# Performance work log

Measured on AMD Instinct MI355X. Metric: run time of the kernel, lower is better.

The kernel has to match this reference:

```python
import jax, jax.numpy as jnp
import numpy as np

N, E, B = 20000, 320000, 64
NODE_DIM, EDGE_DIM, H, T = 64, 32, 128, 256
L = 5            # propagation_depth
DELTA = 1.0      # avg_d['log']
N_AGG, N_SCAL = 4, 3


def _w(k, shape):
    return jax.random.normal(k, shape, jnp.float32) / np.sqrt(shape[-2])


def setup_inputs() -> dict:
    key = jax.random.key(0)
    ks = jax.random.split(key, 12)
    return {
        "node_feat": jax.random.normal(ks[0], (N, NODE_DIM), jnp.float32),
        "edge_feat": jax.random.normal(ks[1], (E, EDGE_DIM), jnp.float32),
        "W_in": _w(ks[2], (NODE_DIM, H)),
        "b_in": jnp.zeros((H,), jnp.float32),
        "pre_W": _w(ks[3], (L, 2 * H + EDGE_DIM, H)),
        "pre_b": jnp.zeros((L, H), jnp.float32),
        "post_W": _w(ks[4], (L, H + N_AGG * N_SCAL * H, H)),
        "post_b": jnp.zeros((L, H), jnp.float32),
        "out_W1": _w(ks[5], (3 * H, H)),
        "out_b1": jnp.zeros((H,), jnp.float32),
        "out_W2": _w(ks[6], (H, T)),
        "out_b2": jnp.zeros((T,), jnp.float32),
        "src": jax.random.randint(ks[7], (E,), 0, N),
        "dst": jax.random.randint(ks[8], (E,), 0, N),
        "node2graph": jnp.sort(jax.random.randint(ks[9], (N,), 0, B)),
    }


def _forward(node_feat, edge_feat, W_in, b_in, pre_W, pre_b, post_W, post_b,
             out_W1, out_b1, out_W2, out_b2, src, dst, node2graph):
    # input node MLP (Linear + ReLU)
    h = jax.nn.relu(node_feat @ W_in + b_in)                       # [N, H]

    # degree-based scalers (constant across layers)
    deg = jax.ops.segment_sum(jnp.ones((E,), h.dtype), dst, num_segments=N)
    has_edge = (deg > 0)[:, None]
    inv_deg = jnp.where(deg > 0, 1.0 / jnp.maximum(deg, 1.0), 0.0)[:, None]
    logd = jnp.log(deg + 1.0)
    amp = (logd / DELTA)[:, None]                                  # amplification
    att = jnp.where(logd > 0, DELTA / jnp.maximum(logd, 1e-12), 1.0)[:, None]

    def step(h, p):
        pW, pb, qW, qb = p
        # pretrans on concat(src feat, dst feat, edge feat)
        m_in = jnp.concatenate([h[src], h[dst], edge_feat], axis=-1)  # [E, 2H+De]
        m = jax.nn.relu(m_in @ pW + pb)                               # [E, H]
        # multi-aggregator gather
        s = jax.ops.segment_sum(m, dst, num_segments=N)
        mean = s * inv_deg
        mx = jnp.where(has_edge, jax.ops.segment_max(m, dst, num_segments=N), 0.0)
        mn = jnp.where(has_edge, jax.ops.segment_min(m, dst, num_segments=N), 0.0)
        agg = jnp.concatenate([mean, mx, mn, s], axis=-1)             # [N, 4H]
        scaled = jnp.concatenate([agg, agg * amp, agg * att], axis=-1)  # [N, 12H]
        # posttrans on concat(h, aggregated)
        h_new = jax.nn.relu(jnp.concatenate([h, scaled], axis=-1) @ qW + qb)
        return h + h_new, None                                        # residual

    h, _ = jax.lax.scan(step, h, (pre_W, pre_b, post_W, post_b))

    # multi-aggregator readout over graphs
    g_sum = jax.ops.segment_sum(h, node2graph, num_segments=B)
    g_cnt = jax.ops.segment_sum(jnp.ones((N, 1), h.dtype), node2graph, num_segments=B)
    g_mean = g_sum / jnp.maximum(g_cnt, 1.0)
    g_max = jnp.where(g_cnt > 0, jax.ops.segment_max(h, node2graph, num_segments=B), 0.0)
    readout = jnp.concatenate([g_mean, g_max, g_sum], axis=-1)        # [B, 3H]
    return jax.nn.relu(readout @ out_W1 + out_b1) @ out_W2 + out_b2   # [B, T]


def reference(node_feat, edge_feat, W_in, b_in, pre_W, pre_b, post_W, post_b,
              out_W1, out_b1, out_W2, out_b2, src, dst, node2graph):
    return _forward(node_feat, edge_feat, W_in, b_in, pre_W, pre_b, post_W, post_b,
                    out_W1, out_b1, out_W2, out_b2, src, dst, node2graph)
```

## Files before the change

kernel.cpp:

```cpp
#include <hip/hip_runtime.h>

#define H 128
#define NODE_DIM 64
#define EDGE_DIM 32
#define KPRE (2*H + EDGE_DIM)
#define KPOST (13*H)
#define T_OUT 256
#define L_DEPTH 5
#define POST_FRAGS (52*8*64)
#define Y_FRAGS (4*16*64)
#define EF_FRAGS (8*64)
#define RCH 8

typedef short short8v __attribute__((ext_vector_type(8)));
typedef float float4v __attribute__((ext_vector_type(4)));

__device__ __forceinline__ unsigned short f2bf(float x) {
    unsigned int b = __float_as_uint(x);
    return (unsigned short)((b + 0x7fffu + ((b >> 16) & 1u)) >> 16);
}
__device__ __forceinline__ float bf2f(unsigned short u) {
    return __uint_as_float((unsigned int)u << 16);
}

__global__ void k_input_mlp(const float* __restrict__ nf, const float* __restrict__ W,
                            const float* __restrict__ b, float* __restrict__ h,
                            unsigned short* __restrict__ h_bf, int N) {
    int gid = blockIdx.x * blockDim.x + threadIdx.x;
    int n = gid >> 7, c = gid & 127;
    if (n >= N) return;
    const float* nrow = nf + (size_t)n * NODE_DIM;
    float acc = 0.f;
#pragma unroll 8
    for (int k = 0; k < NODE_DIM; ++k)
        acc += nrow[k] * W[k * H + c];
    acc += b[c];
    acc = fmaxf(acc, 0.f);
    h[(size_t)n * H + c] = acc;
    h_bf[(size_t)n * H + c] = f2bf(acc);
}

__global__ void k_hist(const int* __restrict__ dst, int* __restrict__ deg_i, int E) {
    int e = blockIdx.x * blockDim.x + threadIdx.x;
    if (e < E) atomicAdd(&deg_i[dst[e]], 1);
}

__global__ __launch_bounds__(1024) void k_scan(const int* __restrict__ deg_i,
                                               int* __restrict__ row_start,
                                               int* __restrict__ cursor, int N) {
    __shared__ int part[1024];
    int t = threadIdx.x;
    int per = (N + 1023) / 1024;
    int base = t * per;
    int s = 0;
    for (int i = 0; i < per; ++i) {
        int idx = base + i;
        if (idx < N) s += deg_i[idx];
    }
    part[t] = s;
    __syncthreads();
    for (int off = 1; off < 1024; off <<= 1) {
        int v = (t >= off) ? part[t - off] : 0;
        __syncthreads();
        part[t] += v;
        __syncthreads();
    }
    int run = (t == 0) ? 0 : part[t - 1];
    for (int i = 0; i < per; ++i) {
        int idx = base + i;
        if (idx < N) {
            row_start[idx] = run;
            cursor[idx] = run;
            run += deg_i[idx];
        }
    }
    if (t == 1023) row_start[N] = run;
}

__global__ void k_sortscatter(const int* __restrict__ src, const int* __restrict__ dst,
                              int* __restrict__ cursor, int* __restrict__ es_src,
                              int* __restrict__ es_eid, int E) {
    int e = blockIdx.x * blockDim.x + threadIdx.x;
    if (e >= E) return;
    int pos = atomicAdd(&cursor[dst[e]], 1);
    es_src[pos] = src[e];
    es_eid[pos] = e;
}

__global__ void k_efsort(const float* __restrict__ ef, const int* __restrict__ es_eid,
                         unsigned short* __restrict__ efs_bf, int E) {
    int t = blockIdx.x * 256 + threadIdx.x;
    int p = t >> 2, q = t & 3;
    if (p >= E) return;
    int eid = es_eid[p];
    const float* sp = ef + (size_t)eid * EDGE_DIM + q * 8;
    float4 v0 = *(const float4*)sp;
    float4 v1 = *(const float4*)(sp + 4);
    short8v o;
    o[0] = (short)f2bf(v0.x); o[1] = (short)f2bf(v0.y);
    o[2] = (short)f2bf(v0.z); o[3] = (short)f2bf(v0.w);
    o[4] = (short)f2bf(v1.x); o[5] = (short)f2bf(v1.y);
    o[6] = (short)f2bf(v1.z); o[7] = (short)f2bf(v1.w);
    *(short8v*)(efs_bf + (size_t)p * EDGE_DIM + q * 8) = o;
}

__global__ void k_scalers(const int* __restrict__ deg_i, float* __restrict__ invd,
                          float* __restrict__ amp, float* __restrict__ att, int N) {
    int n = blockIdx.x * blockDim.x + threadIdx.x;
    if (n >= N) return;
    float d = (float)deg_i[n];
    invd[n] = (d > 0.f) ? (1.f / d) : 0.f;
    float ld = logf(d + 1.f);
    amp[n] = ld;
    att[n] = (d > 0.f) ? (1.f / ld) : 1.f;
}

__global__ void k_gbounds(const int* __restrict__ n2g, int* __restrict__ g_start,
                          int N, int B) {
    int n = blockIdx.x * 256 + threadIdx.x;
    if (n > N) return;
    int cur = (n < N) ? n2g[n] : B;
    int prev = (n == 0) ? -1 : n2g[n - 1];
    for (int g = prev + 1; g <= cur && g <= B; ++g)
        g_start[g] = n;
}

__global__ void k_wconv_all(const float* __restrict__ pre_W,
                            const float* __restrict__ post_W,
                            short* __restrict__ wf_y_all,
                            short* __restrict__ wf_post_all,
                            short* __restrict__ wf_ef_all) {
    const int wrow[13] = {0, 256, 384, 512, 768, 896, 1024, 1280, 1408, 1536, 128, 640, 1152};
    int t = blockIdx.x * 256 + threadIdx.x;
    if (t < L_DEPTH * POST_FRAGS) {
        int l = t / POST_FRAGS, tt = t - l * POST_FRAGS;
        const float* qW = post_W + (size_t)l * KPOST * H;
        int lane = tt & 63, fc = tt >> 6;
        int b = fc >> 5, ks = (fc >> 3) & 3, cb = fc & 7;
        int col = cb * 16 + (lane & 15);
        int k0 = wrow[b] + ks * 32 + ((lane >> 4) << 3);
        short8v o;
#pragma unroll
        for (int j = 0; j < 8; ++j)
            o[j] = (short)f2bf(qW[(size_t)(k0 + j) * H + col]);
        *(short8v*)(wf_post_all + (size_t)t * 8) = o;
        return;
    }
    t -= L_DEPTH * POST_FRAGS;
    if (t < L_DEPTH * Y_FRAGS) {
        int l = t / Y_FRAGS, tt = t - l * Y_FRAGS;
        const float* pW = pre_W + (size_t)l * KPRE * H;
        int lane = tt & 63, fc = tt >> 6;
        int kglob = fc >> 4, cb = fc & 15;
        int col = cb * 16 + (lane & 15);
        int k0 = kglob * 32 + ((lane >> 4) << 3);
        int rowoff = (col < 128) ? 0 : 128;
        int c = col & 127;
        short8v o;
#pragma unroll
        for (int j = 0; j < 8; ++j)
            o[j] = (short)f2bf(pW[(size_t)(rowoff + k0 + j) * H + c]);
        *(short8v*)(wf_y_all + (size_t)t * 8) = o;
        return;
    }
    t -= L_DEPTH * Y_FRAGS;
    if (t >= L_DEPTH * EF_FRAGS) return;
    int l = t / EF_FRAGS, tt = t - l * EF_FRAGS;
    int lane = tt & 63, cb = tt >> 6;
    int col = cb * 16 + (lane & 15);
    int k0 = (lane >> 4) << 3;
    const float* pW = pre_W + (size_t)l * KPRE * H;
    short8v o;
#pragma unroll
    for (int j = 0; j < 8; ++j)
        o[j] = (short)f2bf(pW[(size_t)(2 * H + k0 + j) * H + col]);
    *(short8v*)(wf_ef_all + (size_t)t * 8) = o;
}

__device__ __forceinline__ void efw_body(
    int blk, const unsigned short* __restrict__ efs_bf,
    const short* __restrict__ WfEf, unsigned short* __restrict__ EFW, int E,
    unsigned short (*buf)[16][128])
{
    int tid = threadIdx.x, lane = tid & 63, w = tid >> 6;
    int p0 = blk * 256 + w * 64;
    short8v bfr[8];
#pragma unroll
    for (int cb = 0; cb < 8; ++cb)
        bfr[cb] = *(const short8v*)(WfEf + (size_t)(cb * 64 + lane) * 8);
#pragma unroll
    for (int t4 = 0; t4 < 4; ++t4) {
        int rowb = p0 + t4 * 16;
        int ar = rowb + (lane & 15);
        short8v a = {};
        if (ar < E)
            a = *(const short8v*)(efs_bf + (size_t)ar * EDGE_DIM + ((lane >> 4) << 3));
        float4v acc[8];
#pragma unroll
        for (int cb = 0; cb < 8; ++cb)
            acc[cb] = __builtin_amdgcn_mfma_f32_16x16x32_bf16(
                a, bfr[cb], (float4v){0.f, 0.f, 0.f, 0.f}, 0, 0, 0);
#pragma unroll
        for (int cb = 0; cb < 8; ++cb)
#pragma unroll
            for (int r = 0; r < 4; ++r)
                buf[w][((lane >> 4) << 2) + r][cb * 16 + (lane & 15)] = f2bf(acc[cb][r]);
#pragma unroll
        for (int j = 0; j < 4; ++j) {
            int lr = (lane >> 4) + j * 4;
            int gr = rowb + lr;
            uint4 v = *(const uint4*)&buf[w][lr][(lane & 15) * 8];
            if (gr < E)
                *(uint4*)(EFW + (size_t)gr * H + (lane & 15) * 8) = v;
        }
    }
}

__global__ __launch_bounds__(256) void k_y0_fat(
    const unsigned short* __restrict__ h_bf, const short* __restrict__ Wf,
    unsigned short* __restrict__ Y1bf, unsigned short* __restrict__ Y2bf, int N,
    const unsigned short* __restrict__ efs_bf, const short* __restrict__ WfEf,
    unsigned short* __restrict__ EFW, int E, int nYBlocks)
{
    __shared__ __align__(16) short Xs[64 * 128];
    __shared__ __align__(16) unsigned short buf[4][16][128];
    if (blockIdx.x >= nYBlocks) {
        efw_body(blockIdx.x - nYBlocks, efs_bf, WfEf, EFW, E, buf);
        return;
    }
    int tid = threadIdx.x;
    int n0 = blockIdx.x * 64;
    int lane = tid & 63, wave = tid >> 6;
    float4v acc[16];
#pragma unroll
    for (int cb = 0; cb < 16; ++cb) acc[cb] = (float4v){0.f, 0.f, 0.f, 0.f};

    int rs = tid >> 4, c0 = (tid & 15) * 8;
#pragma unroll
    for (int j = 0; j < 4; ++j) {
        int r = rs + j * 16;
        int n = n0 + r;
        uint4 v = make_uint4(0, 0, 0, 0);
        if (n < N) v = *(const uint4*)(h_bf + (size_t)n * H + c0);
        *(uint4*)((char*)Xs + r * 256 + ((c0 * 2) ^ ((r & 7) << 4))) = v;
    }
    __syncthreads();
    int rloc = wave * 16 + (lane & 15);
    int swz = (rloc & 7) << 4;
#pragma unroll
    for (int ks = 0; ks < 4; ++ks) {
        int boff = rloc * 256 + (((ks * 64) + ((lane >> 4) << 4)) ^ swz);
        short8v a = *(short8v*)((char*)Xs + boff);
        const short* wp = Wf + ((size_t)(ks * 16) * 64 + lane) * 8;
#pragma unroll
        for (int cb = 0; cb < 16; ++cb) {
            short8v b = *(const short8v*)(wp + (size_t)cb * 512);
            acc[cb] = __builtin_amdgcn_mfma_f32_16x16x32_bf16(a, b, acc[cb], 0, 0, 0);
        }
    }
    int col0 = lane & 15;
    int row0 = wave * 16 + ((lane >> 4) << 2);
#pragma unroll
    for (int cb = 0; cb < 16; ++cb) {
        int col = cb * 16 + col0;
#pragma unroll
        for (int r = 0; r < 4; ++r) {
            int n = n0 + row0 + r;
            if (n < N) {
                if (col < 128) Y1bf[(size_t)n * H + col] = f2bf(acc[cb][r]);
                else           Y2bf[(size_t)n * H + (col - 128)] = f2bf(acc[cb][r]);
            }
        }
    }
}

__global__ __launch_bounds__(256) void k_edge_agg(
    const unsigned short* __restrict__ Y1bf, const unsigned short* __restrict__ Y2bf,
    const unsigned short* __restrict__ EFW, const float* __restrict__ pb,
    const int* __restrict__ es_src, const int* __restrict__ row_start,
    unsigned short* __restrict__ s_out, unsigned short* __restrict__ mx_out,
    unsigned short* __restrict__ mn_out, int N)
{
    int tid = threadIdx.x, lane = tid & 63, w = tid >> 6;
    int n = blockIdx.x * 4 + w;
    if (n >= N) return;
    int start = row_start[n], end = row_start[n + 1];
    bool any = end > start;
    unsigned int y2u = *(const unsigned int*)(Y2bf + (size_t)n * H + 2 * lane);
    float2 pbv = *(const float2*)(pb + 2 * lane);
    float y20 = bf2f((unsigned short)(y2u & 0xffffu)) + pbv.x;
    float y21 = bf2f((unsigned short)(y2u >> 16)) + pbv.y;
    float s0 = 0.f, s1 = 0.f;
    float mx0 = any ? -3.4e38f : 0.f, mx1 = any ? -3.4e38f : 0.f;
    float mn0 = any ? 3.4e38f : 0.f,  mn1 = any ? 3.4e38f : 0.f;
#pragma unroll 2
    for (int p = start; p < end; ++p) {
        int sn = __builtin_amdgcn_readfirstlane(es_src[p]);
        unsigned int y1u = *(const unsigned int*)(Y1bf + (size_t)sn * H + 2 * lane);
        unsigned int eu  = *(const unsigned int*)(EFW + (size_t)p * H + 2 * lane);
        float m0 = fmaxf(bf2f((unsigned short)(y1u & 0xffffu)) +
                         bf2f((unsigned short)(eu & 0xffffu)) + y20, 0.f);
        float m1 = fmaxf(bf2f((unsigned short)(y1u >> 16)) +
                         bf2f((unsigned short)(eu >> 16)) + y21, 0.f);
        s0 += m0; s1 += m1;
        mx0 = fmaxf(mx0, m0); mx1 = fmaxf(mx1, m1);
        mn0 = fminf(mn0, m0); mn1 = fminf(mn1, m1);
    }
    size_t o = (size_t)n * H + 2 * lane;
    *(unsigned int*)(s_out + o)  = (unsigned int)f2bf(s0)  | ((unsigned int)f2bf(s1)  << 16);
    *(unsigned int*)(mx_out + o) = (unsigned int)f2bf(mx0) | ((unsigned int)f2bf(mx1) << 16);
    *(unsigned int*)(mn_out + o) = (unsigned int)f2bf(mn0) | ((unsigned int)f2bf(mn1) << 16);
}

__global__ __launch_bounds__(256) void k_post_fat(
    float* __restrict__ h, unsigned short* __restrict__ h_bf,
    const unsigned short* __restrict__ s_in, const unsigned short* __restrict__ mx_in,
    const unsigned short* __restrict__ mn_in,
    const float* __restrict__ invd, const float* __restrict__ amp,
    const float* __restrict__ att,
    const short* __restrict__ Wf, const float* __restrict__ qb,
    const short* __restrict__ WfY, unsigned short* __restrict__ Y1bf,
    unsigned short* __restrict__ Y2bf, int doY, int N,
    const unsigned short* __restrict__ efs_bf, const short* __restrict__ WfEf,
    unsigned short* __restrict__ EFW, int E, int nPostBlocks)
{
    __shared__ __align__(16) short Xs[32 * 128];
    __shared__ __align__(16) unsigned short buf[4][16][128];
    if (blockIdx.x >= nPostBlocks) {
        efw_body(blockIdx.x - nPostBlocks, efs_bf, WfEf, EFW, E, buf);
        return;
    }
    int tid = threadIdx.x, lane = tid & 63, wave = tid >> 6;
    int rh = wave & 1, ch = wave >> 1;
    int n0 = blockIdx.x * 32;

    const unsigned short* const srcs[13] = {h_bf, mx_in, mn_in, s_in, mx_in, mn_in, s_in,
                                            mx_in, mn_in, s_in, s_in, s_in, s_in};
    const int grp_of[13] = {0, 0, 0, 0, 1, 1, 1, 2, 2, 2, 3, 4, 5};

    float4v acc[6][4];
#pragma unroll
    for (int g = 0; g < 6; ++g)
#pragma unroll
        for (int cb = 0; cb < 4; ++cb) acc[g][cb] = (float4v){0.f, 0.f, 0.f, 0.f};

    int arow = n0 + rh * 16 + (lane & 15);
    bool aok = arow < N;
    size_t abase = (size_t)arow * H + ((lane >> 4) << 3);

#pragma unroll
    for (int b = 0; b < 13; ++b) {
        const unsigned short* sp = srcs[b];
#pragma unroll
        for (int ks = 0; ks < 4; ++ks) {
            short8v a = {};
            if (aok) a = *(const short8v*)(sp + abase + ks * 32);
#pragma unroll
            for (int cb = 0; cb < 4; ++cb) {
                short8v bfrag = *(const short8v*)(
                    Wf + ((size_t)((b * 4 + ks) * 8 + ch * 4 + cb) * 64 + lane) * 8);
                acc[grp_of[b]][cb] =
                    __builtin_amdgcn_mfma_f32_16x16x32_bf16(a, bfrag, acc[grp_of[b]][cb], 0, 0, 0);
            }
        }
    }

    int col0 = lane & 15;
    int row0 = rh * 16 + ((lane >> 4) << 2);
    float s_invd[4], s_amp[4], s_att[4];
#pragma unroll
    for (int r = 0; r < 4; ++r) {
        int n = n0 + row0 + r;
        bool ok = n < N;
        s_invd[r] = ok ? invd[n] : 0.f;
        s_amp[r]  = ok ? amp[n]  : 0.f;
        s_att[r]  = ok ? att[n]  : 0.f;
    }
#pragma unroll
    for (int cb = 0; cb < 4; ++cb) {
        int col = (ch * 4 + cb) * 16 + col0;
        float bb = qb[col];
#pragma unroll
        for (int r = 0; r < 4; ++r) {
            int n = n0 + row0 + r;
            if (n < N) {
                float v = acc[0][cb][r]
                        + s_amp[r] * acc[1][cb][r] + s_att[r] * acc[2][cb][r]
                        + s_invd[r] * (acc[3][cb][r] + s_amp[r] * acc[4][cb][r]
                                       + s_att[r] * acc[5][cb][r]);
                size_t o = (size_t)n * H + col;
                float nv = h[o] + fmaxf(v + bb, 0.f);
                h[o] = nv;
                unsigned short us = f2bf(nv);
                h_bf[o] = us;
                if (doY) {
                    int rr = row0 + r;
                    *(short*)((char*)Xs + rr * 256 + ((col * 2) ^ ((rr & 7) << 4))) = (short)us;
                }
            }
        }
    }
    if (doY) {
        __syncthreads();
        float4v yacc[8];
#pragma unroll
        for (int i = 0; i < 8; ++i) yacc[i] = (float4v){0.f, 0.f, 0.f, 0.f};
#pragma unroll
        for (int t16 = 0; t16 < 2; ++t16) {
            int rloc = t16 * 16 + (lane & 15);
            int swz = (rloc & 7) << 4;
#pragma unroll
            for (int ks = 0; ks < 4; ++ks) {
                int boff = rloc * 256 + (((ks * 64) + ((lane >> 4) << 4)) ^ swz);
                short8v a = *(short8v*)((char*)Xs + boff);
#pragma unroll
                for (int cb = 0; cb < 4; ++cb) {
                    const short* wp = WfY + ((size_t)(ks * 16 + wave * 4 + cb) * 64 + lane) * 8;
                    short8v b = *(const short8v*)wp;
                    yacc[t16 * 4 + cb] =
                        __builtin_amdgcn_mfma_f32_16x16x32_bf16(a, b, yacc[t16 * 4 + cb], 0, 0, 0);
                }
            }
        }
#pragma unroll
        for (int t16 = 0; t16 < 2; ++t16) {
#pragma unroll
            for (int cb = 0; cb < 4; ++cb) {
                int col = (wave * 4 + cb) * 16 + col0;
                int r0 = t16 * 16 + ((lane >> 4) << 2);
#pragma unroll
                for (int r = 0; r < 4; ++r) {
                    int n = n0 + r0 + r;
                    if (n < N) {
                        unsigned short v = f2bf(yacc[t16 * 4 + cb][r]);
                        if (col < 128) Y1bf[(size_t)n * H + col] = v;
                        else           Y2bf[(size_t)n * H + (col - 128)] = v;
                    }
                }
            }
        }
    }
}

__global__ __launch_bounds__(256) void k_readout_part(
    const float* __restrict__ h, const int* __restrict__ g_start,
    float* __restrict__ psum, float* __restrict__ pmax, int B)
{
    __shared__ float rs[2][128], rm[2][128];
    int blk = blockIdx.x;
    int b = blk / RCH, chunk = blk % RCH;
    int tid = threadIdx.x;
    int c = tid & 127, half = tid >> 7;
    int g0 = g_start[b], g1 = g_start[b + 1];
    int cnt = g1 - g0;
    int per = (cnt + RCH - 1) / RCH;
    int n0 = g0 + chunk * per;
    int n1 = min(n0 + per, g1);
    float s = 0.f, m = -3.4e38f;
    for (int n = n0 + half; n < n1; n += 2) {
        float v = h[(size_t)n * H + c];
        s += v;
        m = fmaxf(m, v);
    }
    rs[half][c] = s;
    rm[half][c] = m;
    __syncthreads();
    if (tid < 128) {
        size_t o = ((size_t)b * RCH + chunk) * H + c;
        psum[o] = rs[0][c] + rs[1][c];
        pmax[o] = fmaxf(rm[0][c], rm[1][c]);
    }
}

__global__ __launch_bounds__(256) void k_readout_final2(
    const float* __restrict__ psum, const float* __restrict__ pmax,
    const int* __restrict__ g_start,
    const float* __restrict__ W1, const float* __restrict__ b1,
    const float* __restrict__ W2, const float* __restrict__ b2,
    float* __restrict__ out)
{
    __shared__ float xv[3 * H];
    __shared__ float hid[H];
    int b = blockIdx.x, tid = threadIdx.x;
    int cnt = g_start[b + 1] - g_start[b];
    if (tid < 128) {
        int c = tid;
        float s = 0.f, m = -3.4e38f;
#pragma unroll
        for (int j = 0; j < RCH; ++j) {
            size_t o = ((size_t)b * RCH + j) * H + c;
            s += psum[o];
            m = fmaxf(m, pmax[o]);
        }
        float rc = 1.f / fmaxf((float)cnt, 1.f);
        xv[c]         = s * rc;
        xv[H + c]     = (cnt > 0) ? m : 0.f;
        xv[2 * H + c] = s;
    }
    __syncthreads();
    if (tid < 128) {
        float acc = 0.f;
        for (int k = 0; k < 3 * H; ++k)
            acc += xv[k] * W1[k * H + tid];
        hid[tid] = fmaxf(acc + b1[tid], 0.f);
    }
    __syncthreads();
    float acc = 0.f;
#pragma unroll 8
    for (int k = 0; k < H; ++k)
        acc += hid[k] * W2[k * T_OUT + tid];
    out[(size_t)b * T_OUT + tid] = acc + b2[tid];
}

extern "C" void kernel_launch(void* const* d_in, const int* in_sizes, int n_in,
                              void* d_out, int out_size, void* d_ws, size_t ws_size,
                              hipStream_t stream) {
    const float* node_feat = (const float*)d_in[0];
    const float* edge_feat = (const float*)d_in[1];
    const float* W_in  = (const float*)d_in[2];
    const float* b_in  = (const float*)d_in[3];
    const float* pre_W = (const float*)d_in[4];
    const float* pre_b = (const float*)d_in[5];
    const float* post_W = (const float*)d_in[6];
    const float* post_b = (const float*)d_in[7];
    const float* out_W1 = (const float*)d_in[8];
    const float* out_b1 = (const float*)d_in[9];
    const float* out_W2 = (const float*)d_in[10];
    const float* out_b2 = (const float*)d_in[11];
    const int* src = (const int*)d_in[12];
    const int* dst = (const int*)d_in[13];
    const int* n2g = (const int*)d_in[14];

    int N = in_sizes[0] / NODE_DIM;
    int E = in_sizes[1] / EDGE_DIM;
    int B = out_size / T_OUT;
    float* out = (float*)d_out;

    float* ws = (float*)d_ws;
    float* h    = ws; ws += (size_t)N * H;
    float* invd = ws; ws += N;
    float* amp  = ws; ws += N;
    float* att  = ws; ws += N;
    float* psum = ws; ws += (size_t)B * RCH * H;
    float* pmax = ws; ws += (size_t)B * RCH * H;
    ws = (float*)(((uintptr_t)ws + 15) & ~(uintptr_t)15);
    unsigned short* h_bf  = (unsigned short*)ws;
    unsigned short* s_buf = h_bf  + (size_t)N * H;
    unsigned short* mx    = s_buf + (size_t)N * H;
    unsigned short* mn    = mx    + (size_t)N * H;
    unsigned short* Y1bf  = mn    + (size_t)N * H;
    unsigned short* Y2bf  = Y1bf  + (size_t)N * H;
    unsigned short* efs_bf = Y2bf + (size_t)N * H;
    unsigned short* EFW    = efs_bf + (size_t)E * EDGE_DIM;
    short* wf_post_all = (short*)(EFW + (size_t)E * H);
    short* wf_y_all    = wf_post_all + (size_t)L_DEPTH * POST_FRAGS * 8;
    short* wf_ef_all   = wf_y_all + (size_t)L_DEPTH * Y_FRAGS * 8;
    int* deg_i     = (int*)(wf_ef_all + (size_t)L_DEPTH * EF_FRAGS * 8);
    int* row_start = deg_i + N;
    int* cursor    = row_start + N + 1;
    int* es_src    = cursor + N;
    int* es_eid    = es_src + E;
    int* g_start   = es_eid + E;

    int nPostBlocks = (N + 31) / 32;
    int nEfBlocks   = (E + 255) / 256;
    int nYBlocks    = (N + 63) / 64;

    k_input_mlp<<<((size_t)N * H + 255) / 256, 256, 0, stream>>>(node_feat, W_in, b_in,
                                                                 h, h_bf, N);

    hipMemsetAsync(deg_i, 0, (size_t)N * sizeof(int), stream);
    k_hist<<<(E + 255) / 256, 256, 0, stream>>>(dst, deg_i, E);
    k_scan<<<1, 1024, 0, stream>>>(deg_i, row_start, cursor, N);
    k_sortscatter<<<(E + 255) / 256, 256, 0, stream>>>(src, dst, cursor, es_src, es_eid, E);
    k_efsort<<<((size_t)E * 4 + 255) / 256, 256, 0, stream>>>(edge_feat, es_eid, efs_bf, E);
    k_scalers<<<(N + 255) / 256, 256, 0, stream>>>(deg_i, invd, amp, att, N);
    k_gbounds<<<(N + 256) / 256, 256, 0, stream>>>(n2g, g_start, N, B);

    {
        int tot = L_DEPTH * (POST_FRAGS + Y_FRAGS + EF_FRAGS);
        k_wconv_all<<<(tot + 255) / 256, 256, 0, stream>>>(pre_W, post_W, wf_y_all,
                                                           wf_post_all, wf_ef_all);
    }

    k_y0_fat<<<nYBlocks + nEfBlocks, 256, 0, stream>>>(
        h_bf, wf_y_all, Y1bf, Y2bf, N, efs_bf, wf_ef_all, EFW, E, nYBlocks);

    for (int l = 0; l < L_DEPTH; ++l) {
        k_edge_agg<<<(N + 3) / 4, 256, 0, stream>>>(
            Y1bf, Y2bf, EFW, pre_b + (size_t)l * H,
            es_src, row_start, s_buf, mx, mn, N);
        int doY = (l < L_DEPTH - 1) ? 1 : 0;
        int grid = nPostBlocks + (doY ? nEfBlocks : 0);
        k_post_fat<<<grid, 256, 0, stream>>>(
            h, h_bf, s_buf, mx, mn, invd, amp, att,
            wf_post_all + (size_t)l * POST_FRAGS * 8, post_b + (size_t)l * H,
            doY ? (wf_y_all + (size_t)(l + 1) * Y_FRAGS * 8) : wf_y_all,
            Y1bf, Y2bf, doY, N,
            efs_bf, doY ? (wf_ef_all + (size_t)(l + 1) * EF_FRAGS * 8) : wf_ef_all,
            EFW, E, nPostBlocks);
    }

    k_readout_part<<<B * RCH, 256, 0, stream>>>(h, g_start, psum, pmax, B);
    k_readout_final2<<<B, 256, 0, stream>>>(psum, pmax, g_start,
                                            out_W1, out_b1, out_W2, out_b2, out);
}
```

Measured before the change: 647.7 us.

## Fuse edge aggregation into post-transform kernel with LDS staging and double-buffered Y/EFW

The per-layer edge aggregation kernel is merged into the post-transform kernel. Each block first computes the sum, max and min aggregates for its 32 nodes into swizzled LDS, then feeds those tiles straight into the MFMA post-GEMM. Because the fused kernel reads this layer's Y1/Y2/EFW while writing the next layer's, those buffers are double-buffered. This removes one launch per layer and the global write and re-read of the three aggregate arrays. In exchange, each block now does a serial per-node gather before its GEMM, and LDS use grows to 32 KB, which may lower occupancy.

```diff
diff --git a/kernel.cpp b/kernel.cpp
--- a/kernel.cpp
+++ b/kernel.cpp
@@ -274,68 +274,70 @@
     }
 }
 
-__global__ __launch_bounds__(256) void k_edge_agg(
+__global__ __launch_bounds__(256) void k_aggpost_fat(
+    float* __restrict__ h, unsigned short* __restrict__ h_bf,
     const unsigned short* __restrict__ Y1bf, const unsigned short* __restrict__ Y2bf,
     const unsigned short* __restrict__ EFW, const float* __restrict__ pb,
     const int* __restrict__ es_src, const int* __restrict__ row_start,
-    unsigned short* __restrict__ s_out, unsigned short* __restrict__ mx_out,
-    unsigned short* __restrict__ mn_out, int N)
-{
-    int tid = threadIdx.x, lane = tid & 63, w = tid >> 6;
-    int n = blockIdx.x * 4 + w;
-    if (n >= N) return;
-    int start = row_start[n], end = row_start[n + 1];
-    bool any = end > start;
-    unsigned int y2u = *(const unsigned int*)(Y2bf + (size_t)n * H + 2 * lane);
-    float2 pbv = *(const float2*)(pb + 2 * lane);
-    float y20 = bf2f((unsigned short)(y2u & 0xffffu)) + pbv.x;
-    float y21 = bf2f((unsigned short)(y2u >> 16)) + pbv.y;
-    float s0 = 0.f, s1 = 0.f;
-    float mx0 = any ? -3.4e38f : 0.f, mx1 = any ? -3.4e38f : 0.f;
-    float mn0 = any ? 3.4e38f : 0.f,  mn1 = any ? 3.4e38f : 0.f;
-#pragma unroll 2
-    for (int p = start; p < end; ++p) {
-        int sn = __builtin_amdgcn_readfirstlane(es_src[p]);
-        unsigned int y1u = *(const unsigned int*)(Y1bf + (size_t)sn * H + 2 * lane);
-        unsigned int eu  = *(const unsigned int*)(EFW + (size_t)p * H + 2 * lane);
-        float m0 = fmaxf(bf2f((unsigned short)(y1u & 0xffffu)) +
-                         bf2f((unsigned short)(eu & 0xffffu)) + y20, 0.f);
-        float m1 = fmaxf(bf2f((unsigned short)(y1u >> 16)) +
-                         bf2f((unsigned short)(eu >> 16)) + y21, 0.f);
-        s0 += m0; s1 += m1;
-        mx0 = fmaxf(mx0, m0); mx1 = fmaxf(mx1, m1);
-        mn0 = fminf(mn0, m0); mn1 = fminf(mn1, m1);
-    }
-    size_t o = (size_t)n * H + 2 * lane;
-    *(unsigned int*)(s_out + o)  = (unsigned int)f2bf(s0)  | ((unsigned int)f2bf(s1)  << 16);
-    *(unsigned int*)(mx_out + o) = (unsigned int)f2bf(mx0) | ((unsigned int)f2bf(mx1) << 16);
-    *(unsigned int*)(mn_out + o) = (unsigned int)f2bf(mn0) | ((unsigned int)f2bf(mn1) << 16);
-}
-
-__global__ __launch_bounds__(256) void k_post_fat(
-    float* __restrict__ h, unsigned short* __restrict__ h_bf,
-    const unsigned short* __restrict__ s_in, const unsigned short* __restrict__ mx_in,
-    const unsigned short* __restrict__ mn_in,
     const float* __restrict__ invd, const float* __restrict__ amp,
     const float* __restrict__ att,
     const short* __restrict__ Wf, const float* __restrict__ qb,
-    const short* __restrict__ WfY, unsigned short* __restrict__ Y1bf,
-    unsigned short* __restrict__ Y2bf, int doY, int N,
+    const short* __restrict__ WfY, unsigned short* __restrict__ Y1o,
+    unsigned short* __restrict__ Y2o, int doY, int N,
     const unsigned short* __restrict__ efs_bf, const short* __restrict__ WfEf,
-    unsigned short* __restrict__ EFW, int E, int nPostBlocks)
+    unsigned short* __restrict__ EFWo, int E, int nPostBlocks)
 {
-    __shared__ __align__(16) short Xs[32 * 128];
-    __shared__ __align__(16) unsigned short buf[4][16][128];
+    __shared__ __align__(16) char smem[32768];
     if (blockIdx.x >= nPostBlocks) {
-        efw_body(blockIdx.x - nPostBlocks, efs_bf, WfEf, EFW, E, buf);
+        efw_body(blockIdx.x - nPostBlocks, efs_bf, WfEf, EFWo, E,
+                 (unsigned short (*)[16][128])smem);
         return;
     }
+    unsigned short* Ss  = (unsigned short*)smem;
+    unsigned short* Smx = Ss + 32 * 128;
+    unsigned short* Smn = Smx + 32 * 128;
+    short* Xs = (short*)(Smn + 32 * 128);
+
     int tid = threadIdx.x, lane = tid & 63, wave = tid >> 6;
+    int n0 = blockIdx.x * 32;
+
+#pragma unroll 1
+    for (int j = 0; j < 8; ++j) {
+        int r = wave * 8 + j;
+        int n = n0 + r;
+        float s0 = 0.f, s1 = 0.f, mx0 = 0.f, mx1 = 0.f, mn0 = 0.f, mn1 = 0.f;
+        if (n < N) {
+            int start = row_start[n], end = row_start[n + 1];
+            bool any = end > start;
+            unsigned int y2u = *(const unsigned int*)(Y2bf + (size_t)n * H + 2 * lane);
+            float2 pbv = *(const float2*)(pb + 2 * lane);
+            float y20 = bf2f((unsigned short)(y2u & 0xffffu)) + pbv.x;
+            float y21 = bf2f((unsigned short)(y2u >> 16)) + pbv.y;
+            mx0 = any ? -3.4e38f : 0.f; mx1 = mx0;
+            mn0 = any ? 3.4e38f : 0.f;  mn1 = mn0;
+#pragma unroll 2
+            for (int p = start; p < end; ++p) {
+                int sn = __builtin_amdgcn_readfirstlane(es_src[p]);
+                unsigned int y1u = *(const unsigned int*)(Y1bf + (size_t)sn * H + 2 * lane);
+                unsigned int eu  = *(const unsigned int*)(EFW + (size_t)p * H + 2 * lane);
+                float m0 = fmaxf(bf2f((unsigned short)(y1u & 0xffffu)) +
+                                 bf2f((unsigned short)(eu & 0xffffu)) + y20, 0.f);
+                float m1 = fmaxf(bf2f((unsigned short)(y1u >> 16)) +
+                                 bf2f((unsigned short)(eu >> 16)) + y21, 0.f);
+                s0 += m0; s1 += m1;
+                mx0 = fmaxf(mx0, m0); mx1 = fmaxf(mx1, m1);
+                mn0 = fminf(mn0, m0); mn1 = fminf(mn1, m1);
+            }
+        }
+        int boff = (r * 256 + lane * 4) ^ ((r & 7) << 4);
+        *(unsigned int*)((char*)Ss + boff)  = (unsigned int)f2bf(s0)  | ((unsigned int)f2bf(s1)  << 16);
+        *(unsigned int*)((char*)Smx + boff) = (unsigned int)f2bf(mx0) | ((unsigned int)f2bf(mx1) << 16);
+        *(unsigned int*)((char*)Smn + boff) = (unsigned int)f2bf(mn0) | ((unsigned int)f2bf(mn1) << 16);
+    }
+    __syncthreads();
+
     int rh = wave & 1, ch = wave >> 1;
-    int n0 = blockIdx.x * 32;
-
-    const unsigned short* const srcs[13] = {h_bf, mx_in, mn_in, s_in, mx_in, mn_in, s_in,
-                                            mx_in, mn_in, s_in, s_in, s_in, s_in};
+    const int src_of[13] = {0, 1, 2, 3, 1, 2, 3, 1, 2, 3, 3, 3, 3};
     const int grp_of[13] = {0, 0, 0, 0, 1, 1, 1, 2, 2, 2, 3, 4, 5};
 
     float4v acc[6][4];
@@ -344,17 +346,27 @@
 #pragma unroll
         for (int cb = 0; cb < 4; ++cb) acc[g][cb] = (float4v){0.f, 0.f, 0.f, 0.f};
 
-    int arow = n0 + rh * 16 + (lane & 15);
+    int arowL = rh * 16 + (lane & 15);
+    int arow = n0 + arowL;
     bool aok = arow < N;
     size_t abase = (size_t)arow * H + ((lane >> 4) << 3);
+    int lswz = (arowL & 7) << 4;
 
 #pragma unroll
     for (int b = 0; b < 13; ++b) {
-        const unsigned short* sp = srcs[b];
 #pragma unroll
         for (int ks = 0; ks < 4; ++ks) {
-            short8v a = {};
-            if (aok) a = *(const short8v*)(sp + abase + ks * 32);
+            short8v a;
+            if (src_of[b] == 0) {
+                short8v t = {};
+                if (aok) t = *(const short8v*)(h_bf + abase + ks * 32);
+                a = t;
+            } else {
+                const unsigned short* lp = (src_of[b] == 1) ? Smx
+                                          : (src_of[b] == 2) ? Smn : Ss;
+                int boff = (arowL * 256 + ks * 64 + ((lane >> 4) << 4)) ^ lswz;
+                a = *(const short8v*)((const char*)lp + boff);
+            }
 #pragma unroll
             for (int cb = 0; cb < 4; ++cb) {
                 short8v bfrag = *(const short8v*)(
@@ -364,6 +376,7 @@
             }
         }
     }
+    __syncthreads();
 
     int col0 = lane & 15;
     int row0 = rh * 16 + ((lane >> 4) << 2);
@@ -433,8 +446,8 @@
                     int n = n0 + r0 + r;
                     if (n < N) {
                         unsigned short v = f2bf(yacc[t16 * 4 + cb][r]);
-                        if (col < 128) Y1bf[(size_t)n * H + col] = v;
-                        else           Y2bf[(size_t)n * H + (col - 128)] = v;
+                        if (col < 128) Y1o[(size_t)n * H + col] = v;
+                        else           Y2o[(size_t)n * H + (col - 128)] = v;
                     }
                 }
             }
@@ -544,15 +557,15 @@
     float* psum = ws; ws += (size_t)B * RCH * H;
     float* pmax = ws; ws += (size_t)B * RCH * H;
     ws = (float*)(((uintptr_t)ws + 15) & ~(uintptr_t)15);
-    unsigned short* h_bf  = (unsigned short*)ws;
-    unsigned short* s_buf = h_bf  + (size_t)N * H;
-    unsigned short* mx    = s_buf + (size_t)N * H;
-    unsigned short* mn    = mx    + (size_t)N * H;
-    unsigned short* Y1bf  = mn    + (size_t)N * H;
-    unsigned short* Y2bf  = Y1bf  + (size_t)N * H;
-    unsigned short* efs_bf = Y2bf + (size_t)N * H;
-    unsigned short* EFW    = efs_bf + (size_t)E * EDGE_DIM;
-    short* wf_post_all = (short*)(EFW + (size_t)E * H);
+    unsigned short* h_bf   = (unsigned short*)ws;
+    unsigned short* Y1a    = h_bf + (size_t)N * H;
+    unsigned short* Y2a    = Y1a  + (size_t)N * H;
+    unsigned short* Y1b    = Y2a  + (size_t)N * H;
+    unsigned short* Y2b    = Y1b  + (size_t)N * H;
+    unsigned short* efs_bf = Y2b  + (size_t)N * H;
+    unsigned short* EFWa   = efs_bf + (size_t)E * EDGE_DIM;
+    unsigned short* EFWb   = EFWa + (size_t)E * H;
+    short* wf_post_all = (short*)(EFWb + (size_t)E * H);
     short* wf_y_all    = wf_post_all + (size_t)L_DEPTH * POST_FRAGS * 8;
     short* wf_ef_all   = wf_y_all + (size_t)L_DEPTH * Y_FRAGS * 8;
     int* deg_i     = (int*)(wf_ef_all + (size_t)L_DEPTH * EF_FRAGS * 8);
@@ -584,21 +597,26 @@
     }
 
     k_y0_fat<<<nYBlocks + nEfBlocks, 256, 0, stream>>>(
-        h_bf, wf_y_all, Y1bf, Y2bf, N, efs_bf, wf_ef_all, EFW, E, nYBlocks);
+        h_bf, wf_y_all, Y1a, Y2a, N, efs_bf, wf_ef_all, EFWa, E, nYBlocks);
 
     for (int l = 0; l < L_DEPTH; ++l) {
-        k_edge_agg<<<(N + 3) / 4, 256, 0, stream>>>(
-            Y1bf, Y2bf, EFW, pre_b + (size_t)l * H,
-            es_src, row_start, s_buf, mx, mn, N);
         int doY = (l < L_DEPTH - 1) ? 1 : 0;
         int grid = nPostBlocks + (doY ? nEfBlocks : 0);
-        k_post_fat<<<grid, 256, 0, stream>>>(
-            h, h_bf, s_buf, mx, mn, invd, amp, att,
+        int cur = l & 1;
+        unsigned short* Y1c = cur ? Y1b : Y1a;
+        unsigned short* Y2c = cur ? Y2b : Y2a;
+        unsigned short* EFWc = cur ? EFWb : EFWa;
+        unsigned short* Y1n = cur ? Y1a : Y1b;
+        unsigned short* Y2n = cur ? Y2a : Y2b;
+        unsigned short* EFWn = cur ? EFWa : EFWb;
+        k_aggpost_fat<<<grid, 256, 0, stream>>>(
+            h, h_bf, Y1c, Y2c, EFWc, pre_b + (size_t)l * H,
+            es_src, row_start, invd, amp, att,
             wf_post_all + (size_t)l * POST_FRAGS * 8, post_b + (size_t)l * H,
             doY ? (wf_y_all + (size_t)(l + 1) * Y_FRAGS * 8) : wf_y_all,
-            Y1bf, Y2bf, doY, N,
+            Y1n, Y2n, doY, N,
             efs_bf, doY ? (wf_ef_all + (size_t)(l + 1) * EF_FRAGS * 8) : wf_ef_all,
-            EFW, E, nPostBlocks);
+            EFWn, E, nPostBlocks);
     }
 
     k_readout_part<<<B * RCH, 256, 0, stream>>>(h, g_start, psum, pmax, B);
```

Measured after the change: 1.175 ms. 81.4% more time.
